# Kernel optimization log

Measured on AMD Instinct MI355X. Metric: run time of the kernel, lower is better.

## Reference

```python
import jax, jax.numpy as jnp
import numpy as np

K = 4  # number of processing steps (init kwarg)


def setup_inputs() -> dict:
    key = jax.random.key(0)
    ks = jax.random.split(key, 6)
    B, S, D = 4096, 8192, 512
    H = D  # hidden_size == input_size (residual h + f_x)
    scale = 1.0 / np.sqrt(H)
    return {
        "f_x": jax.random.normal(ks[0], (B, D), dtype=jnp.float32),
        "g_S": jax.random.normal(ks[1], (S, D), dtype=jnp.float32),
        # LSTM step: input f_x (size D), 'hidden' is concat([h, r]) of size 2H
        "W_ih": jax.random.uniform(ks[2], (4 * H, D), jnp.float32, -scale, scale),
        "W_hh": jax.random.uniform(ks[3], (4 * H, 2 * H), jnp.float32, -scale, scale),
        "b_ih": jax.random.uniform(ks[4], (4 * H,), jnp.float32, -scale, scale),
        "b_hh": jax.random.uniform(ks[5], (4 * H,), jnp.float32, -scale, scale),
    }


def _lstm_step(x, hidden, c, W_ih, W_hh, b_ih, b_hh):
    # gates: [B, 4H]; PyTorch LSTMCell gate order (i, f, g, o)
    gates = x @ W_ih.T + b_ih + hidden @ W_hh.T + b_hh
    i, f, g, o = jnp.split(gates, 4, axis=1)
    c_new = jax.nn.sigmoid(f) * c + jax.nn.sigmoid(i) * jnp.tanh(g)
    h_new = jax.nn.sigmoid(o) * jnp.tanh(c_new)
    return h_new, c_new


def reference(f_x, g_S, W_ih, W_hh, b_ih, b_hh):
    # f_x: [B, D] queries; g_S: [S, D] support set embeddings
    h = f_x
    c = jnp.zeros_like(f_x)
    for _ in range(K):
        a = jax.nn.softmax(h @ g_S.T, axis=1)       # [B, S] attention over support
        r = a @ g_S                                  # [B, D] attention readout
        concat = jnp.concatenate([h, r], axis=1)     # [B, 2D]
        h, c = _lstm_step(f_x, concat, c, W_ih, W_hh, b_ih, b_hh)
        h = h + f_x                                  # residual skip connection
    return h
```

## Files before the change

### kernel.cpp

```cpp
#include <hip/hip_runtime.h>

typedef _Float16 f16x8 __attribute__((ext_vector_type(8)));
typedef _Float16 f16x4 __attribute__((ext_vector_type(4)));
typedef float f32x4 __attribute__((ext_vector_type(4)));

#define S_DIM 8192
#define D_DIM 512

__device__ __forceinline__ void gload_lds16(const _Float16* g, _Float16* l) {
  __builtin_amdgcn_global_load_lds(
      (const __attribute__((address_space(1))) unsigned int*)g,
      (__attribute__((address_space(3))) unsigned int*)l, 16, 0, 0);
}

__device__ __forceinline__ float sigf(float x) { return 1.0f / (1.0f + __expf(-x)); }
__device__ __forceinline__ float tanhfast(float x) {
  return 1.0f - 2.0f / (__expf(2.0f * x) + 1.0f);
}


template <int BM, int BN>
__global__ __launch_bounds__(256) void gemm_bt(const _Float16* __restrict__ A, int lda,
                                               const _Float16* __restrict__ B, int ldb,
                                               _Float16* __restrict__ C, int ldc, int K) {
  constexpr int BK = 64;
  constexpr int FM = BM / 32, FN = BN / 32;
  __shared__ _Float16 As[BM * BK];
  __shared__ _Float16 Bs[BN * BK];
  const int tid = threadIdx.x;
  const int lane = tid & 63;
  const int wv = tid >> 6;
  const int bm = blockIdx.y * BM;
  const int bn = blockIdx.x * BN;
  const int wm = (wv >> 1) * (BM / 2);
  const int wn = (wv & 1) * (BN / 2);
  const int fr = lane & 15;
  const int hi4 = lane >> 4;
  const int rx7 = fr & 7;
  const int srow = lane >> 3;
  const int schk = (lane & 7) ^ srow;

  f32x4 acc[FM][FN] = {};

  for (int kt = 0; kt < K; kt += BK) {
    __syncthreads();
#pragma unroll
    for (int p = 0; p < BM / 32; ++p) {
      const int m = wv + 4 * p;
      gload_lds16(A + (size_t)(bm + 8 * m + srow) * lda + kt + schk * 8, As + 512 * m);
    }
#pragma unroll
    for (int p = 0; p < BN / 32; ++p) {
      const int m = wv + 4 * p;
      gload_lds16(B + (size_t)(bn + 8 * m + srow) * ldb + kt + schk * 8, Bs + 512 * m);
    }
    __syncthreads();

#pragma unroll
    for (int h = 0; h < 2; ++h) {
      const int co = (((h << 2) | hi4) ^ rx7) << 3;
      f16x8 af[FM], bf[FN];
#pragma unroll
      for (int i = 0; i < FM; ++i)
        af[i] = *(const f16x8*)&As[(wm + i * 16 + fr) * 64 + co];
#pragma unroll
      for (int j = 0; j < FN; ++j)
        bf[j] = *(const f16x8*)&Bs[(wn + j * 16 + fr) * 64 + co];
#pragma unroll
      for (int i = 0; i < FM; ++i)
#pragma unroll
        for (int j = 0; j < FN; ++j)
          acc[i][j] = __builtin_amdgcn_mfma_f32_16x16x32_f16(af[i], bf[j], acc[i][j], 0, 0, 0);
    }
  }

  const int cc = lane & 15;
  const int cr = (lane >> 4) * 4;
#pragma unroll
  for (int i = 0; i < FM; ++i)
#pragma unroll
    for (int j = 0; j < FN; ++j) {
      size_t base = (size_t)(bm + wm + i * 16 + cr) * ldc + (bn + wn + j * 16 + cc);
#pragma unroll
      for (int r = 0; r < 4; ++r) C[base + (size_t)r * ldc] = (_Float16)acc[i][j][r];
    }
}

__global__ __launch_bounds__(256) void gemm_rsplit(const _Float16* __restrict__ A,
                                                   const _Float16* __restrict__ B,
                                                   float* __restrict__ Ppart) {
  constexpr int BK = 64;
  __shared__ _Float16 As[64 * BK];
  __shared__ _Float16 Bs[64 * BK];
  const int tid = threadIdx.x;
  const int lane = tid & 63;
  const int wv = tid >> 6;
  const int bm = blockIdx.x * 64;
  const int bn = blockIdx.y * 64;
  const int kc = blockIdx.z;
  const int k0 = kc * 1024;
  const int wm = (wv >> 1) * 32;
  const int wn = (wv & 1) * 32;
  const int fr = lane & 15;
  const int hi4 = lane >> 4;
  const int rx7 = fr & 7;
  const int srow = lane >> 3;
  const int schk = (lane & 7) ^ srow;

  f32x4 acc[2][2] = {};

  for (int kt = k0; kt < k0 + 1024; kt += BK) {
    __syncthreads();
#pragma unroll
    for (int p = 0; p < 2; ++p) {
      const int m = wv + 4 * p;
      gload_lds16(A + (size_t)(bm + 8 * m + srow) * 16384 + kt + schk * 8, As + 512 * m);
      gload_lds16(B + (size_t)(bn + 8 * m + srow) * 8192 + kt + schk * 8, Bs + 512 * m);
    }
    __syncthreads();

#pragma unroll
    for (int h = 0; h < 2; ++h) {
      const int co = (((h << 2) | hi4) ^ rx7) << 3;
      f16x8 af[2], bf[2];
#pragma unroll
      for (int i = 0; i < 2; ++i) {
        af[i] = *(const f16x8*)&As[(wm + i * 16 + fr) * 64 + co];
        bf[i] = *(const f16x8*)&Bs[(wn + i * 16 + fr) * 64 + co];
      }
#pragma unroll
      for (int i = 0; i < 2; ++i)
#pragma unroll
        for (int j = 0; j < 2; ++j)
          acc[i][j] = __builtin_amdgcn_mfma_f32_16x16x32_f16(af[i], bf[j], acc[i][j], 0, 0, 0);
    }
  }

  const int cc = lane & 15;
  const int cr = (lane >> 4) * 4;
#pragma unroll
  for (int i = 0; i < 2; ++i)
#pragma unroll
    for (int j = 0; j < 2; ++j) {
      size_t base = (size_t)(bm + wm + i * 16 + cr) * 8192 + 4096 + (size_t)kc * 512 +
                    (bn + wn + j * 16 + cc);
#pragma unroll
      for (int r = 0; r < 4; ++r) Ppart[base + (size_t)r * 8192] = acc[i][j][r];
    }
}

__global__ __launch_bounds__(256) void reduce_r(const float* __restrict__ Ppart,
                                                _Float16* __restrict__ rout) {
  int idx = blockIdx.x * 256 + threadIdx.x;
  int m = idx >> 7;
  int n4 = (idx & 127) * 4;
  const float* base = Ppart + (size_t)m * 8192 + 4096 + n4;
  f32x4 s = {0.f, 0.f, 0.f, 0.f};
#pragma unroll
  for (int kc = 0; kc < 8; ++kc) s += *(const f32x4*)(base + kc * 512);
  f16x4 h = {(_Float16)s[0], (_Float16)s[1], (_Float16)s[2], (_Float16)s[3]};
  *(f16x4*)&rout[(size_t)m * 1024 + n4] = h;
}

__global__ __launch_bounds__(256) void gemm_scores(const _Float16* __restrict__ Ah, int ldah,
                                                   const _Float16* __restrict__ Al,
                                                   const _Float16* __restrict__ Bh,
                                                   float* __restrict__ C) {
  constexpr int BK = 64;
  __shared__ _Float16 AsH[128 * BK];
  __shared__ _Float16 AsL[128 * BK];
  __shared__ _Float16 BsH[128 * BK];
  const int tid = threadIdx.x;
  const int lane = tid & 63;
  const int wv = tid >> 6;
  const int bm = blockIdx.y * 128;
  const int bn = blockIdx.x * 128;
  const int wm = (wv >> 1) * 64;
  const int wn = (wv & 1) * 64;
  const int fr = lane & 15;
  const int hi4 = lane >> 4;
  const int rx7 = fr & 7;
  const int srow = lane >> 3;
  const int schk = (lane & 7) ^ srow;

  f32x4 acc[4][4] = {};

  for (int kt = 0; kt < 512; kt += BK) {
    __syncthreads();
#pragma unroll
    for (int p = 0; p < 4; ++p) {
      const int m = wv + 4 * p;
      const int row = 8 * m + srow;
      gload_lds16(Ah + (size_t)(bm + row) * ldah + kt + schk * 8, AsH + 512 * m);
      gload_lds16(Al + (size_t)(bm + row) * 512 + kt + schk * 8, AsL + 512 * m);
      gload_lds16(Bh + (size_t)(bn + row) * 512 + kt + schk * 8, BsH + 512 * m);
    }
    __syncthreads();

#pragma unroll
    for (int h = 0; h < 2; ++h) {
      const int co = (((h << 2) | hi4) ^ rx7) << 3;
      f16x8 fah[4], fal[4], fbh[4];
#pragma unroll
      for (int i = 0; i < 4; ++i) {
        fah[i] = *(const f16x8*)&AsH[(wm + i * 16 + fr) * 64 + co];
        fal[i] = *(const f16x8*)&AsL[(wm + i * 16 + fr) * 64 + co];
        fbh[i] = *(const f16x8*)&BsH[(wn + i * 16 + fr) * 64 + co];
      }
#pragma unroll
      for (int i = 0; i < 4; ++i)
#pragma unroll
        for (int j = 0; j < 4; ++j) {
          acc[i][j] = __builtin_amdgcn_mfma_f32_16x16x32_f16(fah[i], fbh[j], acc[i][j], 0, 0, 0);
          acc[i][j] = __builtin_amdgcn_mfma_f32_16x16x32_f16(fal[i], fbh[j], acc[i][j], 0, 0, 0);
        }
    }
  }

  const int cc = lane & 15;
  const int cr = (lane >> 4) * 4;
#pragma unroll
  for (int i = 0; i < 4; ++i)
#pragma unroll
    for (int j = 0; j < 4; ++j) {
      size_t base = (size_t)(bm + wm + i * 16 + cr) * 8192 + (bn + wn + j * 16 + cc);
#pragma unroll
      for (int r = 0; r < 4; ++r) C[base + (size_t)r * 8192] = acc[i][j][r];
    }
}

__global__ __launch_bounds__(256) void prep_g(const float* __restrict__ g,
                                              _Float16* __restrict__ gT,
                                              _Float16* __restrict__ g_h) {
  __shared__ _Float16 tile[64][72];
  const int s0 = blockIdx.x * 64;
  const int d0 = blockIdx.y * 64;
  const int t = threadIdx.x;
  const int r = t >> 2;
  const int cq = (t & 3) * 16;
  alignas(16) _Float16 buf[16];
#pragma unroll
  for (int q = 0; q < 4; ++q) {
    f32x4 v = *(const f32x4*)&g[(size_t)(s0 + r) * D_DIM + d0 + cq + q * 4];
#pragma unroll
    for (int e = 0; e < 4; ++e) buf[q * 4 + e] = (_Float16)v[e];
  }
#pragma unroll
  for (int k = 0; k < 16; ++k) tile[r][cq + k] = buf[k];
  *(f16x8*)&g_h[(size_t)(s0 + r) * D_DIM + d0 + cq] = *(const f16x8*)&buf[0];
  *(f16x8*)&g_h[(size_t)(s0 + r) * D_DIM + d0 + cq + 8] = *(const f16x8*)&buf[8];
  __syncthreads();
  alignas(16) _Float16 ob[16];
#pragma unroll
  for (int k = 0; k < 16; ++k) ob[k] = tile[cq + k][r];
  *(f16x8*)&gT[(size_t)(d0 + r) * S_DIM + s0 + cq] = *(const f16x8*)&ob[0];
  *(f16x8*)&gT[(size_t)(d0 + r) * S_DIM + s0 + cq + 8] = *(const f16x8*)&ob[8];
}

__global__ __launch_bounds__(256) void prep_misc(const float* __restrict__ W_ih,
                                                 const float* __restrict__ W_hh,
                                                 const float* __restrict__ f_x,
                                                 _Float16* __restrict__ wih_h,
                                                 _Float16* __restrict__ whh_h,
                                                 _Float16* __restrict__ concat,
                                                 _Float16* __restrict__ h_lo,
                                                 float* __restrict__ c) {
  const int NW1 = 2048 * 512 / 4;
  const int NW2 = 2048 * 1024 / 4;
  const int NFX = 4096 * 512 / 4;
  int idx = blockIdx.x * 256 + threadIdx.x;
  if (idx < NW1) {
    f32x4 v = ((const f32x4*)W_ih)[idx];
    f16x4 h = {(_Float16)v[0], (_Float16)v[1], (_Float16)v[2], (_Float16)v[3]};
    ((f16x4*)wih_h)[idx] = h;
  } else if (idx < NW1 + NW2) {
    int k = idx - NW1;
    f32x4 v = ((const f32x4*)W_hh)[k];
    f16x4 h = {(_Float16)v[0], (_Float16)v[1], (_Float16)v[2], (_Float16)v[3]};
    ((f16x4*)whh_h)[k] = h;
  } else if (idx < NW1 + NW2 + NFX) {
    int k = idx - NW1 - NW2;
    f32x4 v = ((const f32x4*)f_x)[k];
    f16x4 h, lo;
#pragma unroll
    for (int e = 0; e < 4; ++e) {
      h[e] = (_Float16)v[e];
      lo[e] = (_Float16)(v[e] - (float)h[e]);
    }
    int m = k >> 7, j4 = k & 127;
    ((f16x4*)concat)[m * 256 + j4] = h;
    ((f16x4*)h_lo)[k] = lo;
    f32x4 z = {0.f, 0.f, 0.f, 0.f};
    ((f32x4*)c)[k] = z;
  }
}

__global__ __launch_bounds__(256) void softmax_inplace(float* __restrict__ P) {
  float* p = P + (size_t)blockIdx.x * S_DIM;
  const int tid = threadIdx.x, lane = tid & 63, wave = tid >> 6;
  __shared__ float red[8];
  float x[32];
#pragma unroll
  for (int i = 0; i < 8; ++i) {
    f32x4 v = *(const f32x4*)&p[i * 1024 + tid * 4];
#pragma unroll
    for (int j = 0; j < 4; ++j) x[i * 4 + j] = v[j];
  }
  float m = -3.0e38f;
#pragma unroll
  for (int k = 0; k < 32; ++k) m = fmaxf(m, x[k]);
#pragma unroll
  for (int o = 32; o; o >>= 1) m = fmaxf(m, __shfl_xor(m, o));
  if (lane == 0) red[wave] = m;
  __syncthreads();
  m = fmaxf(fmaxf(red[0], red[1]), fmaxf(red[2], red[3]));
  float s = 0.f;
#pragma unroll
  for (int k = 0; k < 32; ++k) {
    x[k] = exp2f((x[k] - m) * 1.44269504f);
    s += x[k];
  }
#pragma unroll
  for (int o = 32; o; o >>= 1) s += __shfl_xor(s, o);
  if (lane == 0) red[4 + wave] = s;
  __syncthreads();
  s = (red[4] + red[5]) + (red[6] + red[7]);
  float inv = 1.0f / s;
  _Float16* out = (_Float16*)p;
#pragma unroll
  for (int i = 0; i < 8; ++i) {
    f16x4 v;
#pragma unroll
    for (int j = 0; j < 4; ++j) v[j] = (_Float16)(x[i * 4 + j] * inv);
    *(f16x4*)&out[i * 1024 + tid * 4] = v;
  }
}

__global__ __launch_bounds__(256) void lstm_step(const _Float16* __restrict__ gmm,
                                                 const _Float16* __restrict__ gbase,
                                                 const float* __restrict__ b_ih,
                                                 const float* __restrict__ b_hh,
                                                 const float* __restrict__ f_x,
                                                 float* __restrict__ c,
                                                 _Float16* __restrict__ concat,
                                                 _Float16* __restrict__ h_lo,
                                                 float* __restrict__ hout) {
  int idx = blockIdx.x * 256 + threadIdx.x;
  int m = idx >> 7;
  int j = (idx & 127) * 4;
  size_t grow = (size_t)m * 2048 + j;
  f16x4 gI = *(const f16x4*)&gmm[grow];
  f16x4 gF = *(const f16x4*)&gmm[grow + 512];
  f16x4 gG = *(const f16x4*)&gmm[grow + 1024];
  f16x4 gO = *(const f16x4*)&gmm[grow + 1536];
  f16x4 aI = *(const f16x4*)&gbase[grow];
  f16x4 aF = *(const f16x4*)&gbase[grow + 512];
  f16x4 aG = *(const f16x4*)&gbase[grow + 1024];
  f16x4 aO = *(const f16x4*)&gbase[grow + 1536];
  f32x4 biI = *(const f32x4*)&b_ih[j];
  f32x4 biF = *(const f32x4*)&b_ih[j + 512];
  f32x4 biG = *(const f32x4*)&b_ih[j + 1024];
  f32x4 biO = *(const f32x4*)&b_ih[j + 1536];
  f32x4 bhI = *(const f32x4*)&b_hh[j];
  f32x4 bhF = *(const f32x4*)&b_hh[j + 512];
  f32x4 bhG = *(const f32x4*)&b_hh[j + 1024];
  f32x4 bhO = *(const f32x4*)&b_hh[j + 1536];
  f32x4 cv = ((const f32x4*)c)[idx];
  f32x4 fx = ((const f32x4*)f_x)[idx];
  f32x4 cn, hn;
  f16x4 h16, l16;
#pragma unroll
  for (int k = 0; k < 4; ++k) {
    float gi = (float)gI[k] + (float)aI[k] + biI[k] + bhI[k];
    float gf = (float)gF[k] + (float)aF[k] + biF[k] + bhF[k];
    float gg = (float)gG[k] + (float)aG[k] + biG[k] + bhG[k];
    float go = (float)gO[k] + (float)aO[k] + biO[k] + bhO[k];
    float ci = sigf(gf) * cv[k] + sigf(gi) * tanhfast(gg);
    float hi = sigf(go) * tanhfast(ci) + fx[k];
    cn[k] = ci;
    hn[k] = hi;
    h16[k] = (_Float16)hi;
    l16[k] = (_Float16)(hi - (float)h16[k]);
  }
  ((f32x4*)c)[idx] = cn;
  ((f32x4*)hout)[idx] = hn;
  ((f16x4*)concat)[m * 256 + (idx & 127)] = h16;
  ((f16x4*)h_lo)[idx] = l16;
}

extern "C" void kernel_launch(void* const* d_in, const int* in_sizes, int n_in,
                              void* d_out, int out_size, void* d_ws, size_t ws_size,
                              hipStream_t stream) {
  const float* f_x = (const float*)d_in[0];
  const float* g_S = (const float*)d_in[1];
  const float* W_ih = (const float*)d_in[2];
  const float* W_hh = (const float*)d_in[3];
  const float* b_ih = (const float*)d_in[4];
  const float* b_hh = (const float*)d_in[5];
  float* hout = (float*)d_out;

  char* w = (char*)d_ws;
  float* P32 = (float*)w;
  _Float16* gates = (_Float16*)w;
  _Float16* gbase = (_Float16*)(w + 67108864);
  _Float16* concat = (_Float16*)(w + 83886080);
  _Float16* g_h = (_Float16*)(w + 92274688);
  _Float16* gT = (_Float16*)(w + 109051904);
  _Float16* wih_h = (_Float16*)(w + 117440512);
  _Float16* whh_h = (_Float16*)(w + 119537664);
  float* c = (float*)(w + 123731968);
  _Float16* h_lo = (_Float16*)(w + 132120576);

  prep_g<<<dim3(S_DIM / 64, D_DIM / 64), 256, 0, stream>>>(g_S, gT, g_h);
  prep_misc<<<5120, 256, 0, stream>>>(W_ih, W_hh, f_x, wih_h, whh_h, concat, h_lo, c);

  gemm_bt<128, 128><<<dim3(2048 / 128, 4096 / 128), 256, 0, stream>>>(
      concat, 1024, wih_h, 512, gbase, 2048, 512);

  for (int it = 0; it < 4; ++it) {
    for (int hb = 0; hb < 2; ++hb) {
      const _Float16* hhi = concat + (size_t)hb * 2048 * 1024;
      const _Float16* hlo = h_lo + (size_t)hb * 2048 * 512;
      gemm_scores<<<dim3(64, 16), 256, 0, stream>>>(hhi, 1024, hlo, g_h, P32);
      softmax_inplace<<<2048, 256, 0, stream>>>(P32);
      gemm_rsplit<<<dim3(32, 8, 8), 256, 0, stream>>>((const _Float16*)P32, gT, P32);
      reduce_r<<<1024, 256, 0, stream>>>(P32, concat + (size_t)hb * 2048 * 1024 + 512);
    }
    gemm_bt<128, 128><<<dim3(2048 / 128, 4096 / 128), 256, 0, stream>>>(
        concat, 1024, whh_h, 1024, gates, 2048, 1024);
    lstm_step<<<2048, 256, 0, stream>>>(gates, gbase, b_ih, b_hh, f_x, c, concat, h_lo, hout);
  }
  (void)in_sizes; (void)n_in; (void)out_size; (void)ws_size;
}
```

Before: 892.9 us.

## Prefetch next K tile into registers to overlap global loads with MFMA

Replaces direct global-to-LDS loads in the three GEMM kernels with register-staged loads. The next K tile is loaded into registers while the current tile is computed, then written to LDS after a barrier. This hides global memory latency behind the matrix instructions, at the cost of extra VGPRs and an extra LDS write pass per tile. Occupancy may drop, especially in the 128x128 kernel that holds three staged fragments.

Result: slower. 942.4 us (+5.5%).

```diff
diff --git a/kernel.cpp b/kernel.cpp
--- a/kernel.cpp
+++ b/kernel.cpp
@@ -6,12 +6,6 @@
 
 #define S_DIM 8192
 #define D_DIM 512
-
-__device__ __forceinline__ void gload_lds16(const _Float16* g, _Float16* l) {
-  __builtin_amdgcn_global_load_lds(
-      (const __attribute__((address_space(1))) unsigned int*)g,
-      (__attribute__((address_space(3))) unsigned int*)l, 16, 0, 0);
-}
 
 __device__ __forceinline__ float sigf(float x) { return 1.0f / (1.0f + __expf(-x)); }
 __device__ __forceinline__ float tanhfast(float x) {
@@ -25,6 +19,7 @@
                                                _Float16* __restrict__ C, int ldc, int K) {
   constexpr int BK = 64;
   constexpr int FM = BM / 32, FN = BN / 32;
+  constexpr int PA = BM / 32, PB = BN / 32;
   __shared__ _Float16 As[BM * BK];
   __shared__ _Float16 Bs[BN * BK];
   const int tid = threadIdx.x;
@@ -40,21 +35,34 @@
   const int srow = lane >> 3;
   const int schk = (lane & 7) ^ srow;
 
+  const _Float16* Ab = A + (size_t)(bm + srow) * lda + schk * 8;
+  const _Float16* Bb = B + (size_t)(bn + srow) * ldb + schk * 8;
+
+  f32x4 ra[PA], rb[PB];
+  auto load_ab = [&](int kt) {
+#pragma unroll
+    for (int p = 0; p < PA; ++p)
+      ra[p] = *(const f32x4*)(Ab + (size_t)(8 * (wv + 4 * p)) * lda + kt);
+#pragma unroll
+    for (int p = 0; p < PB; ++p)
+      rb[p] = *(const f32x4*)(Bb + (size_t)(8 * (wv + 4 * p)) * ldb + kt);
+  };
+  auto write_ab = [&]() {
+#pragma unroll
+    for (int p = 0; p < PA; ++p) *((f32x4*)(As + 512 * (wv + 4 * p)) + lane) = ra[p];
+#pragma unroll
+    for (int p = 0; p < PB; ++p) *((f32x4*)(Bs + 512 * (wv + 4 * p)) + lane) = rb[p];
+  };
+
   f32x4 acc[FM][FN] = {};
 
+  load_ab(0);
+  write_ab();
+  __syncthreads();
+
   for (int kt = 0; kt < K; kt += BK) {
-    __syncthreads();
-#pragma unroll
-    for (int p = 0; p < BM / 32; ++p) {
-      const int m = wv + 4 * p;
-      gload_lds16(A + (size_t)(bm + 8 * m + srow) * lda + kt + schk * 8, As + 512 * m);
-    }
-#pragma unroll
-    for (int p = 0; p < BN / 32; ++p) {
-      const int m = wv + 4 * p;
-      gload_lds16(B + (size_t)(bn + 8 * m + srow) * ldb + kt + schk * 8, Bs + 512 * m);
-    }
-    __syncthreads();
+    const bool more = (kt + BK) < K;
+    if (more) load_ab(kt + BK);
 
 #pragma unroll
     for (int h = 0; h < 2; ++h) {
@@ -71,6 +79,11 @@
 #pragma unroll
         for (int j = 0; j < FN; ++j)
           acc[i][j] = __builtin_amdgcn_mfma_f32_16x16x32_f16(af[i], bf[j], acc[i][j], 0, 0, 0);
+    }
+    __syncthreads();
+    if (more) {
+      write_ab();
+      __syncthreads();
     }
   }
 
@@ -107,17 +120,34 @@
   const int srow = lane >> 3;
   const int schk = (lane & 7) ^ srow;
 
+  const _Float16* Ab = A + (size_t)(bm + srow) * 16384 + schk * 8;
+  const _Float16* Bb = B + (size_t)(bn + srow) * 8192 + schk * 8;
+
+  f32x4 ra[2], rb[2];
+  auto load_ab = [&](int kt) {
+#pragma unroll
+    for (int p = 0; p < 2; ++p) {
+      ra[p] = *(const f32x4*)(Ab + (size_t)(8 * (wv + 4 * p)) * 16384 + kt);
+      rb[p] = *(const f32x4*)(Bb + (size_t)(8 * (wv + 4 * p)) * 8192 + kt);
+    }
+  };
+  auto write_ab = [&]() {
+#pragma unroll
+    for (int p = 0; p < 2; ++p) {
+      *((f32x4*)(As + 512 * (wv + 4 * p)) + lane) = ra[p];
+      *((f32x4*)(Bs + 512 * (wv + 4 * p)) + lane) = rb[p];
+    }
+  };
+
   f32x4 acc[2][2] = {};
 
+  load_ab(k0);
+  write_ab();
+  __syncthreads();
+
   for (int kt = k0; kt < k0 + 1024; kt += BK) {
-    __syncthreads();
-#pragma unroll
-    for (int p = 0; p < 2; ++p) {
-      const int m = wv + 4 * p;
-      gload_lds16(A + (size_t)(bm + 8 * m + srow) * 16384 + kt + schk * 8, As + 512 * m);
-      gload_lds16(B + (size_t)(bn + 8 * m + srow) * 8192 + kt + schk * 8, Bs + 512 * m);
-    }
-    __syncthreads();
+    const bool more = (kt + BK) < (k0 + 1024);
+    if (more) load_ab(kt + BK);
 
 #pragma unroll
     for (int h = 0; h < 2; ++h) {
@@ -133,6 +163,11 @@
 #pragma unroll
         for (int j = 0; j < 2; ++j)
           acc[i][j] = __builtin_amdgcn_mfma_f32_16x16x32_f16(af[i], bf[j], acc[i][j], 0, 0, 0);
+    }
+    __syncthreads();
+    if (more) {
+      write_ab();
+      __syncthreads();
     }
   }
 
@@ -183,19 +218,39 @@
   const int srow = lane >> 3;
   const int schk = (lane & 7) ^ srow;
 
-  f32x4 acc[4][4] = {};
-
-  for (int kt = 0; kt < 512; kt += BK) {
-    __syncthreads();
+  const _Float16* Ahb = Ah + (size_t)(bm + srow) * ldah + schk * 8;
+  const _Float16* Alb = Al + (size_t)(bm + srow) * 512 + schk * 8;
+  const _Float16* Bhb = Bh + (size_t)(bn + srow) * 512 + schk * 8;
+
+  f32x4 rah[4], ral[4], rbh[4];
+  auto load_all = [&](int kt) {
+#pragma unroll
+    for (int p = 0; p < 4; ++p) {
+      const size_t m8 = (size_t)(8 * (wv + 4 * p));
+      rah[p] = *(const f32x4*)(Ahb + m8 * ldah + kt);
+      ral[p] = *(const f32x4*)(Alb + m8 * 512 + kt);
+      rbh[p] = *(const f32x4*)(Bhb + m8 * 512 + kt);
+    }
+  };
+  auto write_all = [&]() {
 #pragma unroll
     for (int p = 0; p < 4; ++p) {
       const int m = wv + 4 * p;
-      const int row = 8 * m + srow;
-      gload_lds16(Ah + (size_t)(bm + row) * ldah + kt + schk * 8, AsH + 512 * m);
-      gload_lds16(Al + (size_t)(bm + row) * 512 + kt + schk * 8, AsL + 512 * m);
-      gload_lds16(Bh + (size_t)(bn + row) * 512 + kt + schk * 8, BsH + 512 * m);
-    }
-    __syncthreads();
+      *((f32x4*)(AsH + 512 * m) + lane) = rah[p];
+      *((f32x4*)(AsL + 512 * m) + lane) = ral[p];
+      *((f32x4*)(BsH + 512 * m) + lane) = rbh[p];
+    }
+  };
+
+  f32x4 acc[4][4] = {};
+
+  load_all(0);
+  write_all();
+  __syncthreads();
+
+  for (int kt = 0; kt < 512; kt += BK) {
+    const bool more = (kt + BK) < 512;
+    if (more) load_all(kt + BK);
 
 #pragma unroll
     for (int h = 0; h < 2; ++h) {
@@ -214,6 +269,11 @@
           acc[i][j] = __builtin_amdgcn_mfma_f32_16x16x32_f16(fah[i], fbh[j], acc[i][j], 0, 0, 0);
           acc[i][j] = __builtin_amdgcn_mfma_f32_16x16x32_f16(fal[i], fbh[j], acc[i][j], 0, 0, 0);
         }
+    }
+    __syncthreads();
+    if (more) {
+      write_all();
+      __syncthreads();
     }
   }
 
```
